# Kernel optimization log

Measured on AMD Instinct MI355X. Metric: run time of the kernel, lower is better.

The kernel has to match this reference:

```python
import jax, jax.numpy as jnp
import numpy as np

B, N, D_IN = 8, 2048, 512
H = 1024          # MLP hidden
D_EMB = 512       # embed output dim
D_ATTN = 256      # attn_layers[-1]; KQ MLP outputs 2*D_ATTN


def setup_inputs() -> dict:
    key = jax.random.key(0)
    ks = jax.random.split(key, 9)
    s = lambda fi, fo: (2.0 / (fi + fo)) ** 0.5
    return {
        "x": jax.random.normal(ks[0], (B, N, D_IN), dtype=jnp.float32),
        # embed MLP: Linear(D_IN,H), ReLU, Linear(H,D_EMB)  (weights stored [in,out])
        "We1": jax.random.normal(ks[1], (D_IN, H), dtype=jnp.float32) * s(D_IN, H),
        "be1": jnp.zeros((H,), dtype=jnp.float32),
        "We2": jax.random.normal(ks[2], (H, D_EMB), dtype=jnp.float32) * s(H, D_EMB),
        "be2": jnp.zeros((D_EMB,), dtype=jnp.float32),
        # KQ MLP: Linear(D_IN,H), ReLU, Linear(H, 2*D_ATTN)
        "Wk1": jax.random.normal(ks[3], (D_IN, H), dtype=jnp.float32) * s(D_IN, H),
        "bk1": jnp.zeros((H,), dtype=jnp.float32),
        "Wk2": jax.random.normal(ks[4], (H, 2 * D_ATTN), dtype=jnp.float32) * s(H, 2 * D_ATTN),
        "bk2": jnp.zeros((2 * D_ATTN,), dtype=jnp.float32),
    }


def reference(x, We1, be1, We2, be2, Wk1, bk1, Wk2, bk2):
    # embed MLP
    embs = jax.nn.relu(x @ We1 + be1) @ We2 + be2            # [B,N,D_EMB]
    # KQ MLP; chunk: first half K, second half Q
    kq = jax.nn.relu(x @ Wk1 + bk1) @ Wk2 + bk2              # [B,N,2*D_ATTN]
    K, Q = kq[..., :D_ATTN], kq[..., D_ATTN:]
    # unscaled attention: softmax(Q K^T) V
    scores = jnp.einsum("bqd,bkd->bqk", Q, K)                # [B,N,N]
    A = jax.nn.softmax(scores, axis=-1)
    return jnp.einsum("bqk,bkd->bqd", A, embs)               # [B,N,D_EMB]
```

## Files before the change

kernel.cpp:

```cpp
#include <hip/hip_runtime.h>
#include <stdint.h>

using fx4   = __attribute__((ext_vector_type(4))) float;
using half8 = __attribute__((ext_vector_type(8))) _Float16;

__device__ __forceinline__ ushort f2h(float x) {
  _Float16 h = (_Float16)x;
  union { _Float16 hv; ushort u; } v; v.hv = h;
  return v.u;
}

__device__ __forceinline__ void gload_lds16(const ushort* g, ushort* l) {
  __builtin_amdgcn_global_load_lds(
      (__attribute__((address_space(1))) const void*)g,
      (__attribute__((address_space(3))) void*)l, 16, 0, 0);
}

#define MFMA16(a, b, c) __builtin_amdgcn_mfma_f32_16x16x32_f16(a, b, c, 0, 0, 0)

__device__ __forceinline__ void gemm_body(
    const ushort* __restrict__ A, int lda,
    const ushort* __restrict__ B, int ldb,
    const float* __restrict__ bias,
    void* __restrict__ C, int ldc,
    int K, int flags, int bx, int by,
    ushort* As, ushort* Bs, ushort* __restrict__ C2 = nullptr)
{
  const int tid  = threadIdx.x;
  const int lane = tid & 63;
  const int wave = tid >> 6;
  const int wm   = (wave >> 1) * 64;
  const int wn   = (wave & 1) * 64;
  const long long bm = (long long)by * 128;
  const long long bn = (long long)bx * 128;

  const int srow = tid >> 2;
  const int skq  = (tid & 3) * 8;
  const ushort* a0 = A + (bm + srow) * lda + skq;
  const ushort* a1 = a0 + 64LL * lda;
  const ushort* b0 = B + (bn + srow) * ldb + skq;
  const ushort* b1 = b0 + 64LL * ldb;
  ushort* lA0 = &As[tid * 8];
  ushort* lA1 = &As[2048 + tid * 8];
  ushort* lB0 = &Bs[tid * 8];
  ushort* lB1 = &Bs[2048 + tid * 8];

  fx4 acc[4][4] = {};
  const ushort* ap = &As[(wm + (lane & 15)) * 32 + (lane >> 4) * 8];
  const ushort* bp = &Bs[(wn + (lane & 15)) * 32 + (lane >> 4) * 8];

  for (int k0 = 0; k0 < K; k0 += 32) {
    gload_lds16(a0, lA0);
    gload_lds16(a1, lA1);
    gload_lds16(b0, lB0);
    gload_lds16(b1, lB1);
    a0 += 32; a1 += 32; b0 += 32; b1 += 32;
    __syncthreads();
    half8 af[4], bv[4];
#pragma unroll
    for (int t = 0; t < 4; ++t) {
      af[t] = *(const half8*)(ap + t * 16 * 32);
      bv[t] = *(const half8*)(bp + t * 16 * 32);
    }
#pragma unroll
    for (int i = 0; i < 4; ++i)
#pragma unroll
      for (int j = 0; j < 4; ++j)
        acc[i][j] = MFMA16(af[i], bv[j], acc[i][j]);
    __syncthreads();
  }

  const int col0 = (int)bn + wn + (lane & 15);
  const int row0 = (int)bm + wm + ((lane >> 4) << 2);

  if (flags & 16) {
    ushort* Ch = (ushort*)C;
#pragma unroll
    for (int j = 0; j < 4; ++j) {
      const int col = col0 + j * 16;
      const float bvv = bias ? bias[col] : 0.0f;
#pragma unroll
      for (int i = 0; i < 4; ++i) {
        const int row = row0 + i * 16;
        ushort4 o;
        o.x = f2h(acc[i][j][0] + bvv);
        o.y = f2h(acc[i][j][1] + bvv);
        o.z = f2h(acc[i][j][2] + bvv);
        o.w = f2h(acc[i][j][3] + bvv);
        *(ushort4*)(Ch + (long long)(row >> 5) * 16384 + (long long)col * 32 + (row & 31)) = o;
      }
    }
    return;
  }

  if (flags & 32) {
    ushort* KTp = (ushort*)C;
#pragma unroll
    for (int j = 0; j < 4; ++j) {
      const int col = col0 + j * 16;
      const float bvv = bias ? bias[col] : 0.0f;
#pragma unroll
      for (int i = 0; i < 4; ++i) {
        const int row = row0 + i * 16;
#pragma unroll
        for (int r = 0; r < 4; ++r) {
          const float v = acc[i][j][r] + bvv;
          if (col < 256) {
            const int tok = row + r;
            const int kk  = col & 31;
            KTp[(long long)(tok >> 5) * 8192 + (col >> 5) * 1024 +
                (tok & 31) * 32 + ((((kk >> 3) ^ (tok & 3)) << 3) | (kk & 7))] = f2h(v);
          } else {
            C2[(long long)(row + r) * 256 + (col - 256)] = f2h(v);
          }
        }
      }
    }
    return;
  }

  float*  Cf = (float*)C;
  ushort* Ch = (ushort*)C;
#pragma unroll
  for (int j = 0; j < 4; ++j) {
    const int col = col0 + j * 16;
    const float bvv = bias ? bias[col] : 0.0f;
#pragma unroll
    for (int i = 0; i < 4; ++i) {
      const long long row = row0 + i * 16;
#pragma unroll
      for (int r = 0; r < 4; ++r) {
        float v = acc[i][j][r] + bvv;
        if (flags & 1) v = fmaxf(v, 0.0f);
        if (flags & 2) Ch[(row + r) * ldc + col] = f2h(v);
        else           Cf[(row + r) * ldc + col] = v;
      }
    }
  }
}

__global__ __launch_bounds__(256)
void gemm_bt(const ushort* __restrict__ A, int lda, long long sA,
             const ushort* __restrict__ B, int ldb, long long sB,
             const float* __restrict__ bias,
             void* __restrict__ C, int ldc, long long sC,
             int K, int flags)
{
  __shared__ ushort As[128 * 32];
  __shared__ ushort Bs[128 * 32];
  const int z = blockIdx.z;
  void* Cz = (flags & 2) ? (void*)((ushort*)C + (long long)z * sC)
                         : (void*)((float*)C + (long long)z * sC);
  gemm_body(A + (long long)z * sA, lda, B + (long long)z * sB, ldb, bias,
            Cz, ldc, K, flags, blockIdx.x, blockIdx.y, As, Bs);
}

__global__ __launch_bounds__(256)
void gemm2_pair(const ushort* __restrict__ H, const ushort* __restrict__ W2c,
                const float* __restrict__ be2, const float* __restrict__ bk2,
                ushort* __restrict__ VT, ushort* __restrict__ KT,
                ushort* __restrict__ Qm)
{
  __shared__ ushort As[128 * 32];
  __shared__ ushort Bs[128 * 32];
  if (blockIdx.z == 0)
    gemm_body(H, 2048, W2c, 1024, be2, VT, 0, 1024, 16,
              blockIdx.x, blockIdx.y, As, Bs);
  else
    gemm_body(H + 1024, 2048, W2c + 524288, 1024, bk2, KT, 0, 1024, 32,
              blockIdx.x, blockIdx.y, As, Bs, Qm);
}

__global__ __launch_bounds__(512, 2)
void attn_fused(const ushort* __restrict__ KT, const ushort* __restrict__ VT,
                const ushort* __restrict__ Qm, float* __restrict__ out)
{
  extern __shared__ char smem[];
  ushort* Kb     = (ushort*)smem;
  ushort* Ps     = (ushort*)(smem + 131072);
  float*  rmax   = (float*)(smem + 151552);
  float*  alphaA = (float*)(smem + 152576);
  float*  lred   = rmax;

  const int tid  = threadIdx.x;
  const int lane = tid & 63;
  const int w    = tid >> 6;
  const int c    = lane & 15;
  const int q4   = lane >> 4;
  const int qw   = w >> 2;
  const int tw   = w & 3;
  const int dw   = w * 64;
  const int z    = blockIdx.x;
  const long long tb = (long long)z * 2048;
  const long long pbase = (long long)z * 64;
  const int q0   = blockIdx.y * 64;

  half8 aq[2][8];
#pragma unroll
  for (int i = 0; i < 2; ++i)
#pragma unroll
    for (int dc = 0; dc < 8; ++dc)
      aq[i][dc] = *(const half8*)(Qm + (tb + q0 + qw * 32 + i * 16 + c) * 256 + dc * 32 + q4 * 8);

  {
    const ushort* src = KT + pbase * 8192;
#pragma unroll
    for (int i = 0; i < 8; ++i) {
      const int chunk = w * 8 + i;
      gload_lds16(src + chunk * 512 + lane * 8, Kb + chunk * 512 + lane * 8);
    }
  }
  __syncthreads();

  float m_reg[2][4], l_part[2][4];
#pragma unroll
  for (int i = 0; i < 2; ++i)
#pragma unroll
    for (int r = 0; r < 4; ++r) { m_reg[i][r] = -3.0e38f; l_part[i][r] = 0.0f; }
  fx4 o[4][4] = {};

  const int swz = (q4 ^ (c & 3)) << 3;

  int cur = 0;
  for (int t0 = 0; t0 < 2048; t0 += 128) {
    const long long pt = pbase + (t0 >> 5);
    half8 vb[4][4];
#pragma unroll
    for (int kc = 0; kc < 4; ++kc)
#pragma unroll
      for (int n = 0; n < 4; ++n)
        vb[kc][n] = *(const half8*)(VT + (pt + kc) * 16384 +
                                    (dw + n * 16 + c) * 32 + q4 * 8);
    {
      const long long ptn = pbase + (((t0 + 128) & 2047) >> 5);
      const ushort* src = KT + ptn * 8192;
      ushort* dst = Kb + (cur ^ 1) * 32768;
#pragma unroll
      for (int i = 0; i < 8; ++i) {
        const int chunk = w * 8 + i;
        gload_lds16(src + chunk * 512 + lane * 8, dst + chunk * 512 + lane * 8);
      }
    }
    const ushort* kp = Kb + cur * 32768 + tw * 8192;
    fx4 s[2][2] = {};
#pragma unroll
    for (int dc = 0; dc < 8; ++dc) {
      const half8 b0 = *(const half8*)(kp + dc * 1024 + c * 32 + swz);
      const half8 b1 = *(const half8*)(kp + dc * 1024 + (16 + c) * 32 + swz);
      s[0][0] = MFMA16(aq[0][dc], b0, s[0][0]); s[0][1] = MFMA16(aq[0][dc], b1, s[0][1]);
      s[1][0] = MFMA16(aq[1][dc], b0, s[1][0]); s[1][1] = MFMA16(aq[1][dc], b1, s[1][1]);
    }
#pragma unroll
    for (int i = 0; i < 2; ++i) {
      fx4 rm;
#pragma unroll
      for (int r = 0; r < 4; ++r) rm[r] = fmaxf(s[i][0][r], s[i][1][r]);
#pragma unroll
      for (int off = 1; off < 16; off <<= 1)
#pragma unroll
        for (int r = 0; r < 4; ++r) rm[r] = fmaxf(rm[r], __shfl_xor(rm[r], off, 64));
      if (c == 0) {
#pragma unroll
        for (int r = 0; r < 4; ++r)
          rmax[tw * 64 + qw * 32 + i * 16 + q4 * 4 + r] = rm[r];
      }
    }
    __syncthreads();
#pragma unroll
    for (int i = 0; i < 2; ++i)
#pragma unroll
      for (int r = 0; r < 4; ++r) {
        const int q = qw * 32 + i * 16 + q4 * 4 + r;
        const float mo = m_reg[i][r];
        float mn = fmaxf(fmaxf(rmax[q], rmax[64 + q]),
                         fmaxf(rmax[128 + q], rmax[192 + q]));
        mn = fmaxf(mn, mo);
        m_reg[i][r] = mn;
        const float a  = __expf(mo - mn);
        const float e0 = __expf(s[i][0][r] - mn);
        const float e1 = __expf(s[i][1][r] - mn);
        l_part[i][r] = a * l_part[i][r] + e0 + e1;
        Ps[tw * 2560 + q * 40 + c]      = f2h(e0);
        Ps[tw * 2560 + q * 40 + 16 + c] = f2h(e1);
        if (tw == 0 && c == 0) alphaA[q] = a;
      }
    __syncthreads();
#pragma unroll
    for (int i4 = 0; i4 < 4; ++i4)
#pragma unroll
      for (int r = 0; r < 4; ++r) {
        const float aq_ = alphaA[i4 * 16 + q4 * 4 + r];
#pragma unroll
        for (int n = 0; n < 4; ++n) o[i4][n][r] *= aq_;
      }
#pragma unroll
    for (int kc = 0; kc < 4; ++kc) {
      half8 pa[4];
#pragma unroll
      for (int i4 = 0; i4 < 4; ++i4)
        pa[i4] = *(const half8*)(Ps + kc * 2560 + (i4 * 16 + c) * 40 + q4 * 8);
#pragma unroll
      for (int i4 = 0; i4 < 4; ++i4)
#pragma unroll
        for (int n = 0; n < 4; ++n)
          o[i4][n] = MFMA16(pa[i4], vb[kc][n], o[i4][n]);
    }
    cur ^= 1;
  }

#pragma unroll
  for (int i = 0; i < 2; ++i) {
    fx4 lv;
#pragma unroll
    for (int r = 0; r < 4; ++r) lv[r] = l_part[i][r];
#pragma unroll
    for (int off = 1; off < 16; off <<= 1)
#pragma unroll
      for (int r = 0; r < 4; ++r) lv[r] += __shfl_xor(lv[r], off, 64);
    if (c == 0) {
#pragma unroll
      for (int r = 0; r < 4; ++r)
        lred[tw * 64 + qw * 32 + i * 16 + q4 * 4 + r] = lv[r];
    }
  }
  __syncthreads();

  float* ob = out + (tb + q0) * 512 + dw;
#pragma unroll
  for (int i4 = 0; i4 < 4; ++i4)
#pragma unroll
    for (int r = 0; r < 4; ++r) {
      const int q = i4 * 16 + q4 * 4 + r;
      const float li = 1.0f / (lred[q] + lred[64 + q] + lred[128 + q] + lred[192 + q]);
#pragma unroll
      for (int n = 0; n < 4; ++n)
        ob[(long long)q * 512 + n * 16 + c] = o[i4][n][r] * li;
    }
}

__global__ __launch_bounds__(256)
void transpose_cast_w2(const float* __restrict__ in0, const float* __restrict__ in1,
                       ushort* __restrict__ out0, ushort* __restrict__ out1,
                       int R, int C) {
  __shared__ float tile[32][33];
  const float* in  = blockIdx.z ? in1 : in0;
  ushort*      outp = blockIdx.z ? out1 : out0;
  const int c0 = blockIdx.x * 32, r0 = blockIdx.y * 32;
  const int tx = threadIdx.x & 31, ty = threadIdx.x >> 5;
#pragma unroll
  for (int i = 0; i < 32; i += 8)
    tile[ty + i][tx] = in[(long long)(r0 + ty + i) * C + (c0 + tx)];
  __syncthreads();
#pragma unroll
  for (int i = 0; i < 32; i += 8)
    outp[(long long)(c0 + ty + i) * R + (r0 + tx)] = f2h(tile[tx][ty + i]);
}

__global__ __launch_bounds__(256)
void cast_f32_f16(const float* __restrict__ in, ushort* __restrict__ out) {
  const long long i = ((long long)blockIdx.x * 256 + threadIdx.x) * 4;
  const float4 v = *(const float4*)(in + i);
  ushort4 o;
  o.x = f2h(v.x); o.y = f2h(v.y); o.z = f2h(v.z); o.w = f2h(v.w);
  *(ushort4*)(out + i) = o;
}

__global__ __launch_bounds__(256)
void concat_bias(const float* __restrict__ b0, const float* __restrict__ b1,
                 float* __restrict__ out) {
  const int i = blockIdx.x * 256 + threadIdx.x;
  out[i] = (i < 1024) ? b0[i] : b1[i - 1024];
}

extern "C" void kernel_launch(void* const* d_in, const int* in_sizes, int n_in,
                              void* d_out, int out_size, void* d_ws, size_t ws_size,
                              hipStream_t stream) {
  (void)in_sizes; (void)n_in; (void)out_size; (void)ws_size;
  const float* x   = (const float*)d_in[0];
  const float* We1 = (const float*)d_in[1];
  const float* be1 = (const float*)d_in[2];
  const float* We2 = (const float*)d_in[3];
  const float* be2 = (const float*)d_in[4];
  const float* Wk1 = (const float*)d_in[5];
  const float* bk1 = (const float*)d_in[6];
  const float* Wk2 = (const float*)d_in[7];
  const float* bk2 = (const float*)d_in[8];
  float* out = (float*)d_out;
  char* ws = (char*)d_ws;

  ushort* Xb  = (ushort*)(ws + 0);
  ushort* W2c = (ushort*)(ws + 0);
  ushort* H   = (ushort*)(ws + 16777216);
  ushort* VT  = (ushort*)(ws + 83886080);
  ushort* KT  = (ushort*)(ws + 100663296);
  ushort* Qm  = (ushort*)(ws + 109051904);
  float*  b1c = (float*)(ws + 117440512);
  ushort* W1c = (ushort*)(ws + 117448704);

  cast_f32_f16<<<dim3(8192), 256, 0, stream>>>(x, Xb);
  transpose_cast_w2<<<dim3(32, 16, 2), 256, 0, stream>>>(We1, Wk1, W1c, W1c + 524288, 512, 1024);
  concat_bias<<<dim3(8), 256, 0, stream>>>(be1, bk1, b1c);

  gemm_bt<<<dim3(16, 128, 1), 256, 0, stream>>>(Xb, 512, 0, W1c, 512, 0, b1c,
                                                H, 2048, 0, 512, 1 | 2);

  transpose_cast_w2<<<dim3(16, 32, 2), 256, 0, stream>>>(We2, Wk2, W2c, W2c + 524288, 1024, 512);

  gemm2_pair<<<dim3(4, 128, 2), 256, 0, stream>>>(H, W2c, be2, bk2, VT, KT, Qm);

  hipFuncSetAttribute(reinterpret_cast<const void*>(attn_fused),
                      hipFuncAttributeMaxDynamicSharedMemorySize, 152832);
  attn_fused<<<dim3(8, 32), 512, 152832, stream>>>(KT, VT, Qm, out);
}
```

Measured before the change: 372.8 us.

## Split V loads around barriers and use soft barriers in fused attention

Replaces __syncthreads in the attention loop with a barrier that waits only on LDS counters, so outstanding global loads (V tiles, async K prefetch) can stay in flight across barriers. The V register loads are split into two halves issued later in the iteration. A partial vmcnt wait guards the K prefetch. Launch bounds drop to one block per CU to free registers, and the K prefetch index pattern becomes contiguous per thread. This trades occupancy for manual latency hiding and risks ordering errors if the vmcnt count is wrong.

```diff
diff --git a/kernel.cpp b/kernel.cpp
--- a/kernel.cpp
+++ b/kernel.cpp
@@ -14,6 +14,12 @@
   __builtin_amdgcn_global_load_lds(
       (__attribute__((address_space(1))) const void*)g,
       (__attribute__((address_space(3))) void*)l, 16, 0, 0);
+}
+
+__device__ __forceinline__ void soft_barrier() {
+  asm volatile("s_waitcnt lgkmcnt(0)" ::: "memory");
+  __builtin_amdgcn_s_barrier();
+  asm volatile("" ::: "memory");
 }
 
 #define MFMA16(a, b, c) __builtin_amdgcn_mfma_f32_16x16x32_f16(a, b, c, 0, 0, 0)
@@ -171,7 +177,7 @@
               blockIdx.x, blockIdx.y, As, Bs, Qm);
 }
 
-__global__ __launch_bounds__(512, 2)
+__global__ __launch_bounds__(512, 1)
 void attn_fused(const ushort* __restrict__ KT, const ushort* __restrict__ VT,
                 const ushort* __restrict__ Qm, float* __restrict__ out)
 {
@@ -194,6 +200,7 @@
   const long long tb = (long long)z * 2048;
   const long long pbase = (long long)z * 64;
   const int q0   = blockIdx.y * 64;
+  const int swz  = (q4 ^ (c & 3)) << 3;
 
   half8 aq[2][8];
 #pragma unroll
@@ -205,10 +212,8 @@
   {
     const ushort* src = KT + pbase * 8192;
 #pragma unroll
-    for (int i = 0; i < 8; ++i) {
-      const int chunk = w * 8 + i;
-      gload_lds16(src + chunk * 512 + lane * 8, Kb + chunk * 512 + lane * 8);
-    }
+    for (int i = 0; i < 8; ++i)
+      gload_lds16(src + (i * 512 + tid) * 8, Kb + (i * 512 + tid) * 8);
   }
   __syncthreads();
 
@@ -218,29 +223,19 @@
 #pragma unroll
     for (int r = 0; r < 4; ++r) { m_reg[i][r] = -3.0e38f; l_part[i][r] = 0.0f; }
   fx4 o[4][4] = {};
-
-  const int swz = (q4 ^ (c & 3)) << 3;
 
   int cur = 0;
   for (int t0 = 0; t0 < 2048; t0 += 128) {
     const long long pt = pbase + (t0 >> 5);
-    half8 vb[4][4];
-#pragma unroll
-    for (int kc = 0; kc < 4; ++kc)
-#pragma unroll
-      for (int n = 0; n < 4; ++n)
-        vb[kc][n] = *(const half8*)(VT + (pt + kc) * 16384 +
-                                    (dw + n * 16 + c) * 32 + q4 * 8);
     {
       const long long ptn = pbase + (((t0 + 128) & 2047) >> 5);
       const ushort* src = KT + ptn * 8192;
       ushort* dst = Kb + (cur ^ 1) * 32768;
 #pragma unroll
-      for (int i = 0; i < 8; ++i) {
-        const int chunk = w * 8 + i;
-        gload_lds16(src + chunk * 512 + lane * 8, dst + chunk * 512 + lane * 8);
-      }
-    }
+      for (int i = 0; i < 8; ++i)
+        gload_lds16(src + (i * 512 + tid) * 8, dst + (i * 512 + tid) * 8);
+    }
+    asm volatile("" ::: "memory");
     const ushort* kp = Kb + cur * 32768 + tw * 8192;
     fx4 s[2][2] = {};
 #pragma unroll
@@ -250,6 +245,13 @@
       s[0][0] = MFMA16(aq[0][dc], b0, s[0][0]); s[0][1] = MFMA16(aq[0][dc], b1, s[0][1]);
       s[1][0] = MFMA16(aq[1][dc], b0, s[1][0]); s[1][1] = MFMA16(aq[1][dc], b1, s[1][1]);
     }
+    half8 vb01[2][4];
+#pragma unroll
+    for (int kc = 0; kc < 2; ++kc)
+#pragma unroll
+      for (int n = 0; n < 4; ++n)
+        vb01[kc][n] = *(const half8*)(VT + (pt + kc) * 16384 +
+                                      (dw + n * 16 + c) * 32 + q4 * 8);
 #pragma unroll
     for (int i = 0; i < 2; ++i) {
       fx4 rm;
@@ -265,7 +267,7 @@
           rmax[tw * 64 + qw * 32 + i * 16 + q4 * 4 + r] = rm[r];
       }
     }
-    __syncthreads();
+    soft_barrier();
 #pragma unroll
     for (int i = 0; i < 2; ++i)
 #pragma unroll
@@ -284,15 +286,23 @@
         Ps[tw * 2560 + q * 40 + 16 + c] = f2h(e1);
         if (tw == 0 && c == 0) alphaA[q] = a;
       }
-    __syncthreads();
+    asm volatile("s_waitcnt vmcnt(8)" ::: "memory");
+    soft_barrier();
 #pragma unroll
     for (int i4 = 0; i4 < 4; ++i4)
 #pragma unroll
       for (int r = 0; r < 4; ++r) {
-        const float aq_ = alphaA[i4 * 16 + q4 * 4 + r];
-#pragma unroll
-        for (int n = 0; n < 4; ++n) o[i4][n][r] *= aq_;
-      }
+        const float aqr = alphaA[i4 * 16 + q4 * 4 + r];
+#pragma unroll
+        for (int n = 0; n < 4; ++n) o[i4][n][r] *= aqr;
+      }
+    half8 vb23[2][4];
+#pragma unroll
+    for (int kc = 0; kc < 2; ++kc)
+#pragma unroll
+      for (int n = 0; n < 4; ++n)
+        vb23[kc][n] = *(const half8*)(VT + (pt + 2 + kc) * 16384 +
+                                      (dw + n * 16 + c) * 32 + q4 * 8);
 #pragma unroll
     for (int kc = 0; kc < 4; ++kc) {
       half8 pa[4];
@@ -303,7 +313,8 @@
       for (int i4 = 0; i4 < 4; ++i4)
 #pragma unroll
         for (int n = 0; n < 4; ++n)
-          o[i4][n] = MFMA16(pa[i4], vb[kc][n], o[i4][n]);
+          o[i4][n] = MFMA16(pa[i4], (kc < 2 ? vb01[kc][n] : vb23[kc - 2][n]),
+                            o[i4][n]);
     }
     cur ^= 1;
   }
@@ -323,7 +334,7 @@
         lred[tw * 64 + qw * 32 + i * 16 + q4 * 4 + r] = lv[r];
     }
   }
-  __syncthreads();
+  soft_barrier();
 
   float* ob = out + (tb + q0) * 512 + dw;
 #pragma unroll
```

Result: faster. 357.4 us (-4.1%).
